# Kernel tuning notes

Measured on AMD Instinct MI355X. Metric: run time of the kernel, lower is better.

The kernel has to match this reference:

```python
import jax, jax.numpy as jnp
import numpy as np

D_MODEL = 1024
N_STATE = 16
D_INNER = 2 * D_MODEL          # 2048
DT_RANK = (D_MODEL + 15) // 16  # 64 = ceil(d/16)
K_CONV = 4
B, L = 1, 1024


def setup_inputs() -> dict:
    key = jax.random.key(0)
    ks = jax.random.split(key, 9)
    s = lambda fan_in: 1.0 / np.sqrt(fan_in)
    x = jax.random.normal(ks[0], (B, L, D_MODEL), dtype=jnp.float32)
    W_in = jax.random.normal(ks[1], (D_MODEL, 2 * D_INNER), dtype=jnp.float32) * s(D_MODEL)
    conv_w = jax.random.normal(ks[2], (D_INNER, K_CONV), dtype=jnp.float32) * s(K_CONV)
    conv_b = jnp.zeros((D_INNER,), dtype=jnp.float32)
    W_x = jax.random.normal(ks[3], (D_INNER, DT_RANK + 2 * N_STATE), dtype=jnp.float32) * s(D_INNER)
    W_dt = jax.random.normal(ks[4], (DT_RANK, D_INNER), dtype=jnp.float32) * s(DT_RANK)
    b_dt = jax.random.normal(ks[5], (D_INNER,), dtype=jnp.float32) * 0.01
    # A_log initialized as log(1..N) repeated over d_inner, as in __init__
    A_log = jnp.log(jnp.broadcast_to(jnp.arange(1, N_STATE + 1, dtype=jnp.float32), (D_INNER, N_STATE)))
    D = jnp.ones((D_INNER,), dtype=jnp.float32)
    W_out = jax.random.normal(ks[6], (D_INNER, D_MODEL), dtype=jnp.float32) * s(D_INNER)
    return {"x": x, "W_in": W_in, "conv_w": conv_w, "conv_b": conv_b,
            "W_x": W_x, "W_dt": W_dt, "b_dt": b_dt, "A_log": A_log,
            "D": D, "W_out": W_out}


def _causal_dw_conv(x, w, b):
    # x: [B,L,C], w: [C,K], b: [C]; causal depthwise conv (pad left K-1)
    K = w.shape[1]
    xp = jnp.pad(x, ((0, 0), (K - 1, 0), (0, 0)))
    Lx = x.shape[1]
    out = b
    for k in range(K):  # small fixed K=4
        out = out + xp[:, k:k + Lx, :] * w[:, k]
    return out


def _selective_scan(u, delta, A, Bm, Cm, D):
    # u,delta: [B,L,Di]; A: [Di,N]; Bm,Cm: [B,L,N]; D: [Di]
    dA = jnp.exp(delta[..., None] * A)                      # [B,L,Di,N]
    dBu = delta[..., None] * Bm[:, :, None, :] * u[..., None]
    dA_t = jnp.moveaxis(dA, 1, 0)    # [L,B,Di,N]
    dBu_t = jnp.moveaxis(dBu, 1, 0)
    C_t = jnp.moveaxis(Cm, 1, 0)     # [L,B,N]

    def step(h, inp):
        dA_i, dBu_i, C_i = inp
        h = dA_i * h + dBu_i
        y = jnp.einsum('bdn,bn->bd', h, C_i)
        return h, y

    h0 = jnp.zeros(u.shape[:1] + A.shape, dtype=u.dtype)  # [B,Di,N]
    _, ys = jax.lax.scan(step, h0, (dA_t, dBu_t, C_t))
    y = jnp.moveaxis(ys, 0, 1)       # [B,L,Di]
    return y + u * D


def reference(x, W_in, conv_w, conv_b, W_x, W_dt, b_dt, A_log, D, W_out):
    silu = jax.nn.silu
    x_and_res = x @ W_in                                   # [B,L,2*Di]
    x_in, res = jnp.split(x_and_res, 2, axis=-1)
    x_conv = silu(_causal_dw_conv(x_in, conv_w, conv_b))   # [B,L,Di]
    x_dbl = x_conv @ W_x                                   # [B,L,dt_rank+2N]
    dt, Bm, Cm = jnp.split(x_dbl, [DT_RANK, DT_RANK + N_STATE], axis=-1)
    delta = jax.nn.softplus(dt @ W_dt + b_dt)              # [B,L,Di]
    A = -jnp.exp(A_log)                                    # [Di,N]
    y = _selective_scan(x_conv, delta, A, Bm, Cm, D)
    return (y * silu(res)) @ W_out                         # [B,L,d_model]
```

## Files before the change

kernel.cpp:

```cpp
#include <hip/hip_runtime.h>

typedef unsigned short u16;
typedef unsigned int u32;
typedef __attribute__((ext_vector_type(8))) short bf16x8;
typedef __attribute__((ext_vector_type(4))) float f32x4;

#define LSEQ 1024
#define NSL 8

__device__ __forceinline__ float b2f(u16 v) { return __uint_as_float(((u32)v) << 16); }
__device__ __forceinline__ u16 f2b(float f) {
    u32 x = __float_as_uint(f);
    return (u16)((x + 0x7fffu + ((x >> 16) & 1u)) >> 16);
}
__device__ __forceinline__ float rdf(const void* p, size_t i, int f) {
    return f ? b2f(((const u16*)p)[i]) : ((const float*)p)[i];
}
__device__ __forceinline__ float fsig(float x) {
    return __builtin_amdgcn_rcpf(1.f + __expf(-x));
}

typedef const __attribute__((address_space(1))) u32* gp_t;
typedef __attribute__((address_space(3))) u32* lp_t;
__device__ __forceinline__ void gload16(const u16* g, u16* lds_wave_base) {
    __builtin_amdgcn_global_load_lds((gp_t)g, (lp_t)lds_wave_base, 16, 0, 0);
}

__global__ __launch_bounds__(256) void prep_k(const void* __restrict__ x,
                                              const void* __restrict__ W_in,
                                              const void* __restrict__ W_out,
                                              const void* __restrict__ W_x,
                                              const void* __restrict__ W_dt,
                                              u16* __restrict__ xb,
                                              u16* __restrict__ W_in_t,
                                              u16* __restrict__ W_out_t,
                                              u16* __restrict__ W_x_t,
                                              u16* __restrict__ W_dt_t,
                                              int* __restrict__ flag) {
    __shared__ int cnt;
    __shared__ __align__(8) u16 tile[32][36];
    if (threadIdx.x == 0) cnt = 0;
    __syncthreads();
    const u16* xu = (const u16*)x;
    int c = 0;
#pragma unroll
    for (int j = 0; j < 8; ++j) {
        u16 u = xu[threadIdx.x * 8 + j];
        int e = (u >> 7) & 0xFF;
        c += (e == 0 || (e >= 100 && e <= 140)) ? 1 : 0;
    }
    atomicAdd(&cnt, c);
    __syncthreads();
    const int f = (cnt >= 1638) ? 1 : 0;
    if (blockIdx.x == 0 && threadIdx.x == 0) *flag = f;

    int blk = blockIdx.x;
    if (blk < 1024) {
        int i = (blk * 256 + threadIdx.x) * 4;
        ushort4 o;
        if (f) {
            o = *(const ushort4*)(xu + i);
        } else {
            float4 v = *(const float4*)((const float*)x + i);
            o = make_ushort4(f2b(v.x), f2b(v.y), f2b(v.z), f2b(v.w));
        }
        *(ushort4*)(xb + i) = o;
        return;
    }
    blk -= 1024;
    const void* src; u16* dst; int R, Cn, nbc, t;
    if (blk < 4096)      { src = W_in;  dst = W_in_t;  R = 1024; Cn = 4096; nbc = 128; t = blk; }
    else if (blk < 6144) { src = W_out; dst = W_out_t; R = 2048; Cn = 1024; nbc = 32;  t = blk - 4096; }
    else if (blk < 6400) { src = W_x;   dst = W_x_t;   R = 2048; Cn = 96;   nbc = 4;   t = blk - 6144; }
    else                 { src = W_dt;  dst = W_dt_t;  R = 64;   Cn = 2048; nbc = 64;  t = blk - 6400; }
    int br = t / nbc, bc = t - br * nbc;
    int r0 = br * 32, c0 = bc * 32;
    {
        int ty = threadIdx.x >> 3, tx4 = (threadIdx.x & 7) << 2;
        u16 o0 = 0, o1 = 0, o2 = 0, o3 = 0;
        if (c0 + tx4 < Cn) {
            size_t off = (size_t)(r0 + ty) * Cn + c0 + tx4;
            if (f) {
                ushort4 u = *(const ushort4*)((const u16*)src + off);
                o0 = u.x; o1 = u.y; o2 = u.z; o3 = u.w;
            } else {
                float4 v = *(const float4*)((const float*)src + off);
                o0 = f2b(v.x); o1 = f2b(v.y); o2 = f2b(v.z); o3 = f2b(v.w);
            }
        }
        *(ushort4*)(&tile[ty][tx4]) = make_ushort4(o0, o1, o2, o3);
    }
    __syncthreads();
    {
        int cc = threadIdx.x >> 3, r4 = (threadIdx.x & 7) << 2;
        ushort4 o = make_ushort4(tile[r4][cc], tile[r4 + 1][cc], tile[r4 + 2][cc], tile[r4 + 3][cc]);
        *(ushort4*)(dst + (size_t)(c0 + cc) * R + r0 + r4) = o;
    }
}

template <int MT, int NT, int OUT_MODE>
__global__ __launch_bounds__(256) void gemm_bt(const u16* __restrict__ A,
                                               const u16* __restrict__ Bt,
                                               void* __restrict__ C,
                                               int M, int N, int K,
                                               const int* __restrict__ flag) {
    constexpr int BM = 32 * MT, BN = 32 * NT;
    __shared__ __align__(16) u16 As[2][2 * BM * 32];
    __shared__ __align__(16) u16 Bs[2][2 * BN * 32];
    const int tid = threadIdx.x;
    const int w = tid >> 6, lane = tid & 63;
    const int wm = w & 1, wn = w >> 1;
    const int m_blk = blockIdx.x * BM, n_blk = blockIdx.y * BN;
    const int lm = lane & 15, lq = lane >> 4;
    const int sr = lane >> 2, sc = (lane & 3) << 3;
    const int f = (OUT_MODE == 2) ? flag[0] : 0;

    f32x4 acc[MT][NT];
#pragma unroll
    for (int i = 0; i < MT; ++i)
#pragma unroll
        for (int j = 0; j < NT; ++j) acc[i][j] = (f32x4){0.f, 0.f, 0.f, 0.f};

    auto stage = [&](int buf, int kb) {
#pragma unroll
        for (int cch = 0; cch < 2; ++cch) {
#pragma unroll
            for (int i = 0; i < BM / 64; ++i) {
                int row = i * 64 + w * 16;
                gload16(A + (size_t)(m_blk + row + sr) * K + kb + cch * 32 + sc,
                        &As[buf][cch * BM * 32 + row * 32]);
            }
#pragma unroll
            for (int i = 0; i < BN / 64; ++i) {
                int row = i * 64 + w * 16;
                gload16(Bt + (size_t)(n_blk + row + sr) * K + kb + cch * 32 + sc,
                        &Bs[buf][cch * BN * 32 + row * 32]);
            }
        }
    };
    auto compute = [&](int buf) {
#pragma unroll
        for (int cch = 0; cch < 2; ++cch) {
            bf16x8 af[MT], bf[NT];
#pragma unroll
            for (int tm = 0; tm < MT; ++tm)
                af[tm] = *(const bf16x8*)(&As[buf][cch * BM * 32 +
                                                   (wm * 16 * MT + tm * 16 + lm) * 32 + lq * 8]);
#pragma unroll
            for (int tn = 0; tn < NT; ++tn)
                bf[tn] = *(const bf16x8*)(&Bs[buf][cch * BN * 32 +
                                                   (wn * 16 * NT + tn * 16 + lm) * 32 + lq * 8]);
#pragma unroll
            for (int tm = 0; tm < MT; ++tm)
#pragma unroll
                for (int tn = 0; tn < NT; ++tn)
                    acc[tm][tn] = __builtin_amdgcn_mfma_f32_16x16x32_bf16(af[tm], bf[tn],
                                                                          acc[tm][tn], 0, 0, 0);
        }
    };

    stage(0, 0);
    __syncthreads();
    int cur = 0;
    for (int kb = 64; kb < K; kb += 64) {
        stage(cur ^ 1, kb);
        compute(cur);
        __syncthreads();
        cur ^= 1;
    }
    compute(cur);

#pragma unroll
    for (int tm = 0; tm < MT; ++tm)
#pragma unroll
        for (int tn = 0; tn < NT; ++tn)
#pragma unroll
            for (int r = 0; r < 4; ++r) {
                int row = m_blk + wm * 16 * MT + tm * 16 + lq * 4 + r;
                int col = n_blk + wn * 16 * NT + tn * 16 + lm;
                float v = acc[tm][tn][r];
                if (OUT_MODE == 1) {
                    ((u16*)C)[(size_t)row * N + col] = f2b(v);
                } else {
                    if (f) ((u16*)C)[(size_t)row * N + col] = f2b(v);
                    else   ((float*)C)[(size_t)row * N + col] = v;
                }
            }
}

__global__ __launch_bounds__(256) void gemm2_conv_k(const u16* __restrict__ xz,
                                                    const u16* __restrict__ Bt,
                                                    float* __restrict__ parts,
                                                    u16* __restrict__ xconv,
                                                    const void* __restrict__ cw,
                                                    const void* __restrict__ cb,
                                                    const int* __restrict__ flag) {
    constexpr int MT = 2, NT = 4;
    constexpr int BM = 64, BN = 128, K = 2048, KLEN = 256;
    __shared__ __align__(16) u16 As[2][2 * BM * 32];
    __shared__ __align__(16) u16 Bs[2][2 * BN * 32];
    __shared__ __align__(16) float cws[KLEN * 4];
    __shared__ float cbs[KLEN];
    const int tid = threadIdx.x;
    const int w = tid >> 6, lane = tid & 63;
    const int wm = w & 1, wn = w >> 1;
    const int m_blk = blockIdx.x * BM;
    const int kb0 = blockIdx.z * KLEN;
    const int lm = lane & 15, lq = lane >> 4;
    const int sr = lane >> 2, sc = (lane & 3) << 3;
    const int f = flag[0];

    {
#pragma unroll
        for (int k = 0; k < 4; ++k) cws[tid * 4 + k] = rdf(cw, (size_t)(kb0 + tid) * 4 + k, f);
        cbs[tid] = rdf(cb, kb0 + tid, f);
    }
    __syncthreads();

    f32x4 acc[MT][NT];
#pragma unroll
    for (int i = 0; i < MT; ++i)
#pragma unroll
        for (int j = 0; j < NT; ++j) acc[i][j] = (f32x4){0.f, 0.f, 0.f, 0.f};

    const int arow = tid >> 2;
    const int acg = (tid & 3) << 3;
    const int trow = m_blk + arow;

    auto bstage = [&](int buf, int kb) {
#pragma unroll
        for (int cch = 0; cch < 2; ++cch)
#pragma unroll
            for (int i = 0; i < BN / 64; ++i) {
                int row = i * 64 + w * 16;
                gload16(Bt + (size_t)(row + sr) * K + kb + cch * 32 + sc,
                        &Bs[buf][cch * BN * 32 + row * 32]);
            }
    };
    auto astage = [&](int buf, int cch, int kbase) {
        const int d = kbase + acg;
        const int dl = kbase - kb0 + acg;
        bf16x8 xv[4];
#pragma unroll
        for (int kk = 0; kk < 4; ++kk) {
            bf16x8 zz = {0, 0, 0, 0, 0, 0, 0, 0};
            int tt = trow + kk - 3;
            xv[kk] = (tt >= 0) ? *(const bf16x8*)(xz + (size_t)tt * 4096 + d) : zz;
        }
        bf16x8 rv;
#pragma unroll
        for (int j = 0; j < 8; ++j) {
            f32x4 wv = *(const f32x4*)(cws + (dl + j) * 4);
            float a = cbs[dl + j];
#pragma unroll
            for (int kk = 0; kk < 4; ++kk) a += b2f((u16)xv[kk][j]) * wv[kk];
            rv[j] = (short)f2b(a * fsig(a));
        }
        *(bf16x8*)(&As[buf][cch * BM * 32 + arow * 32 + acg]) = rv;
        *(bf16x8*)(xconv + (size_t)trow * 2048 + d) = rv;
    };
    auto compute = [&](int buf) {
#pragma unroll
        for (int cch = 0; cch < 2; ++cch) {
            bf16x8 af[MT], bf[NT];
#pragma unroll
            for (int tm = 0; tm < MT; ++tm)
                af[tm] = *(const bf16x8*)(&As[buf][cch * BM * 32 +
                                                   (wm * 32 + tm * 16 + lm) * 32 + lq * 8]);
#pragma unroll
            for (int tn = 0; tn < NT; ++tn)
                bf[tn] = *(const bf16x8*)(&Bs[buf][cch * BN * 32 +
                                                   (wn * 64 + tn * 16 + lm) * 32 + lq * 8]);
#pragma unroll
            for (int tm = 0; tm < MT; ++tm)
#pragma unroll
                for (int tn = 0; tn < NT; ++tn)
                    acc[tm][tn] = __builtin_amdgcn_mfma_f32_16x16x32_bf16(af[tm], bf[tn],
                                                                          acc[tm][tn], 0, 0, 0);
        }
    };

    bstage(0, kb0);
    astage(0, 0, kb0);
    astage(0, 1, kb0 + 32);
    __syncthreads();
    int cur = 0;
    for (int kb = kb0 + 64; kb < kb0 + KLEN; kb += 64) {
        bstage(cur ^ 1, kb);
        astage(cur ^ 1, 0, kb);
        astage(cur ^ 1, 1, kb + 32);
        compute(cur);
        __syncthreads();
        cur ^= 1;
    }
    compute(cur);

#pragma unroll
    for (int tm = 0; tm < MT; ++tm)
#pragma unroll
        for (int tn = 0; tn < NT; ++tn)
#pragma unroll
            for (int r = 0; r < 4; ++r) {
                int row = m_blk + wm * 32 + tm * 16 + lq * 4 + r;
                int col = wn * 64 + tn * 16 + lm;
                parts[(size_t)blockIdx.z * 131072 + (size_t)row * 128 + col] = acc[tm][tn][r];
            }
}

__device__ __forceinline__ void delta_tile(const float* __restrict__ parts,
                                           const u16* __restrict__ Wdt,
                                           const void* __restrict__ bias,
                                           int f, int t0, int d0,
                                           u16* As2, u16* Bs2, float (*dlt)[128],
                                           int tid, int w, int lm, int lq, int sr, int sc) {
#pragma unroll
    for (int cch = 0; cch < 2; ++cch)
#pragma unroll
        for (int i = 0; i < 2; ++i) {
            int row = i * 64 + w * 16;
            gload16(Wdt + (size_t)(d0 + row + sr) * 64 + cch * 32 + sc,
                    Bs2 + cch * 4096 + row * 32);
        }
    {
        int arow = tid >> 3, acg = (tid & 7) << 3;
        f32x4 s0 = {0.f, 0.f, 0.f, 0.f}, s1 = {0.f, 0.f, 0.f, 0.f};
#pragma unroll
        for (int sl = 0; sl < NSL; ++sl) {
            const float* p = parts + (size_t)sl * 131072 + (size_t)(t0 + arow) * 128 + acg;
            s0 += *(const f32x4*)p;
            s1 += *(const f32x4*)(p + 4);
        }
        bf16x8 rv;
#pragma unroll
        for (int j = 0; j < 4; ++j) {
            rv[j] = (short)f2b(s0[j]);
            rv[4 + j] = (short)f2b(s1[j]);
        }
        *(bf16x8*)(As2 + (acg >> 5) * 1024 + arow * 32 + (acg & 31)) = rv;
    }
    __syncthreads();

    f32x4 dacc[2][2];
#pragma unroll
    for (int i = 0; i < 2; ++i)
#pragma unroll
        for (int j = 0; j < 2; ++j) dacc[i][j] = (f32x4){0.f, 0.f, 0.f, 0.f};
#pragma unroll
    for (int cch = 0; cch < 2; ++cch) {
        bf16x8 af[2], bf[2];
#pragma unroll
        for (int tm = 0; tm < 2; ++tm)
            af[tm] = *(const bf16x8*)(As2 + cch * 1024 + (tm * 16 + lm) * 32 + lq * 8);
#pragma unroll
        for (int tn = 0; tn < 2; ++tn)
            bf[tn] = *(const bf16x8*)(Bs2 + cch * 4096 + (w * 32 + tn * 16 + lm) * 32 + lq * 8);
#pragma unroll
        for (int tm = 0; tm < 2; ++tm)
#pragma unroll
            for (int tn = 0; tn < 2; ++tn)
                dacc[tm][tn] = __builtin_amdgcn_mfma_f32_16x16x32_bf16(af[tm], bf[tn],
                                                                       dacc[tm][tn], 0, 0, 0);
    }
#pragma unroll
    for (int tm = 0; tm < 2; ++tm)
#pragma unroll
        for (int tn = 0; tn < 2; ++tn)
#pragma unroll
            for (int r = 0; r < 4; ++r) {
                int row = tm * 16 + lq * 4 + r;
                int col = w * 32 + tn * 16 + lm;
                float b = rdf(bias, d0 + col, f);
                float t2 = dacc[tm][tn][r] + b;
                dlt[row][col] = fmaxf(t2, 0.f) + __logf(1.f + __expf(-fabsf(t2)));
            }
    __syncthreads();
}

__global__ __launch_bounds__(256) void scan1_k(const u16* __restrict__ xc,
                                               const float* __restrict__ parts,
                                               const u16* __restrict__ Wdt,
                                               const void* __restrict__ bias,
                                               const void* __restrict__ A_log,
                                               float* __restrict__ Acar,
                                               float* __restrict__ Bcar,
                                               const int* __restrict__ flag) {
    __shared__ __align__(16) u16 As2[2 * 32 * 32];
    __shared__ __align__(16) u16 Bs2[2 * 128 * 32];
    __shared__ float dlt[32][128];
    __shared__ float BCs[32][32];
    const int f = *flag;
    const int tid = threadIdx.x, b = blockIdx.x;
    const int w = tid >> 6, lane = tid & 63;
    const int lm = lane & 15, lq = lane >> 4;
    const int sr = lane >> 2, sc = (lane & 3) << 3;
    const int c = b >> 4;
    const int d0 = (b & 15) * 128;
    const int t0 = c * 32;
    {
        int idx = tid * 4;
        int tl = idx >> 5, col = idx & 31;
        f32x4 s = {0.f, 0.f, 0.f, 0.f};
#pragma unroll
        for (int sl = 0; sl < NSL; ++sl)
            s += *(const f32x4*)(parts + (size_t)sl * 131072 + (size_t)(t0 + tl) * 128 + 64 + col);
        *(f32x4*)&BCs[tl][col] = s;
    }
    delta_tile(parts, Wdt, bias, f, t0, d0, As2, Bs2, dlt, tid, w, lm, lq, sr, sc);

    const int dl = tid >> 1, nh = tid & 1;
    const int d = d0 + dl, n0 = nh << 3;
    float A[8], P[8], h[8];
#pragma unroll
    for (int j = 0; j < 8; ++j) {
        A[j] = -__expf(rdf(A_log, d * 16 + n0 + j, f));
        P[j] = 1.f;
        h[j] = 0.f;
    }
#pragma unroll 4
    for (int i = 0; i < 32; ++i) {
        int t = t0 + i;
        float de = dlt[i][dl];
        float dBu = de * b2f(xc[t * 2048 + d]);
        f32x4 Bv0 = *(const f32x4*)&BCs[i][n0];
        f32x4 Bv1 = *(const f32x4*)&BCs[i][n0 + 4];
#pragma unroll
        for (int j = 0; j < 8; ++j) {
            float Bv = (j < 4) ? Bv0[j & 3] : Bv1[j & 3];
            float a = __expf(de * A[j]);
            h[j] = a * h[j] + Bv * dBu;
            P[j] *= a;
        }
    }
    f32x4 pa0 = {P[0], P[1], P[2], P[3]}, pa1 = {P[4], P[5], P[6], P[7]};
    f32x4 hb0 = {h[0], h[1], h[2], h[3]}, hb1 = {h[4], h[5], h[6], h[7]};
    size_t base = (size_t)c * 32768 + d * 16 + n0;
    *(f32x4*)(Acar + base) = pa0;
    *(f32x4*)(Acar + base + 4) = pa1;
    *(f32x4*)(Bcar + base) = hb0;
    *(f32x4*)(Bcar + base + 4) = hb1;
}

__global__ __launch_bounds__(64) void scan2_k(const float* __restrict__ Acar,
                                              float* __restrict__ Bcar) {
    int idx = blockIdx.x * 64 + threadIdx.x;
    float a[32], b[32];
#pragma unroll
    for (int c = 0; c < 32; ++c) {
        a[c] = Acar[c * 32768 + idx];
        b[c] = Bcar[c * 32768 + idx];
    }
    float H = 0.f;
#pragma unroll
    for (int c = 0; c < 32; ++c) {
        float t = b[c];
        b[c] = H;
        H = a[c] * H + t;
    }
#pragma unroll
    for (int c = 0; c < 32; ++c) Bcar[c * 32768 + idx] = b[c];
}

__global__ __launch_bounds__(256) void scan3_k(const u16* __restrict__ xc,
                                               const float* __restrict__ parts,
                                               const u16* __restrict__ Wdt,
                                               const void* __restrict__ bias,
                                               const u16* __restrict__ xz,
                                               const void* __restrict__ A_log,
                                               const void* __restrict__ Dvp,
                                               const float* __restrict__ Bcar,
                                               u16* __restrict__ yg,
                                               const int* __restrict__ flag) {
    __shared__ __align__(16) u16 As2[2 * 32 * 32];
    __shared__ __align__(16) u16 Bs2[2 * 128 * 32];
    __shared__ float dlt[32][128];
    __shared__ float BCs[32][32];
    const int f = *flag;
    const int tid = threadIdx.x, b = blockIdx.x;
    const int w = tid >> 6, lane = tid & 63;
    const int lm = lane & 15, lq = lane >> 4;
    const int sr = lane >> 2, sc = (lane & 3) << 3;
    const int c = b >> 4;
    const int d0 = (b & 15) * 128;
    const int t0 = c * 32;
    {
        int idx = tid * 4;
        int tl = idx >> 5, col = idx & 31;
        f32x4 s = {0.f, 0.f, 0.f, 0.f};
#pragma unroll
        for (int sl = 0; sl < NSL; ++sl)
            s += *(const f32x4*)(parts + (size_t)sl * 131072 + (size_t)(t0 + tl) * 128 + 64 + col);
        *(f32x4*)&BCs[tl][col] = s;
    }
    delta_tile(parts, Wdt, bias, f, t0, d0, As2, Bs2, dlt, tid, w, lm, lq, sr, sc);

    const int dl = tid >> 1, nh = tid & 1;
    const int d = d0 + dl, n0 = nh << 3;
    float A[8], h[8];
    size_t base = (size_t)c * 32768 + d * 16 + n0;
    f32x4 h0 = *(const f32x4*)(Bcar + base);
    f32x4 h1 = *(const f32x4*)(Bcar + base + 4);
#pragma unroll
    for (int j = 0; j < 8; ++j) {
        A[j] = -__expf(rdf(A_log, d * 16 + n0 + j, f));
        h[j] = (j < 4) ? h0[j & 3] : h1[j & 3];
    }
    float Dd = rdf(Dvp, d, f);
#pragma unroll 4
    for (int i = 0; i < 32; ++i) {
        int t = t0 + i;
        float de = dlt[i][dl];
        float u = b2f(xc[t * 2048 + d]);
        float dBu = de * u;
        f32x4 Bv0 = *(const f32x4*)&BCs[i][n0];
        f32x4 Bv1 = *(const f32x4*)&BCs[i][n0 + 4];
        f32x4 Cv0 = *(const f32x4*)&BCs[i][16 + n0];
        f32x4 Cv1 = *(const f32x4*)&BCs[i][20 + n0];
        float p = 0.f;
#pragma unroll
        for (int j = 0; j < 8; ++j) {
            float Bv = (j < 4) ? Bv0[j & 3] : Bv1[j & 3];
            float Cv = (j < 4) ? Cv0[j & 3] : Cv1[j & 3];
            float a = __expf(de * A[j]);
            h[j] = a * h[j] + Bv * dBu;
            p += h[j] * Cv;
        }
        p += __shfl_xor(p, 1);
        if (nh == 0) {
            float r = b2f(xz[(size_t)t * 4096 + 2048 + d]);
            float yt = p + u * Dd;
            yg[t * 2048 + d] = f2b(yt * r * fsig(r));
        }
    }
}

__global__ __launch_bounds__(256) void gemm3_red_k(const float* __restrict__ parts,
                                                   const u16* __restrict__ Bt,
                                                   float* __restrict__ delta,
                                                   const void* __restrict__ bias,
                                                   const int* __restrict__ flag) {
    constexpr int MT = 2, NT = 2, BM = 64, BN = 64, K = 64;
    __shared__ __align__(16) u16 As[2 * BM * 32];
    __shared__ __align__(16) u16 Bs[2 * BN * 32];
    const int tid = threadIdx.x;
    const int w = tid >> 6, lane = tid & 63;
    const int wm = w & 1, wn = w >> 1;
    const int m_blk = blockIdx.x * BM, n_blk = blockIdx.y * BN;
    const int lm = lane & 15, lq = lane >> 4;
    const int sr = lane >> 2, sc = (lane & 3) << 3;
    const int f = flag[0];

    f32x4 acc[MT][NT];
#pragma unroll
    for (int i = 0; i < MT; ++i)
#pragma unroll
        for (int j = 0; j < NT; ++j) acc[i][j] = (f32x4){0.f, 0.f, 0.f, 0.f};

    const int arow = tid >> 2;
    const int acg = (tid & 3) << 3;

#pragma unroll
    for (int cch = 0; cch < 2; ++cch) {
        int row = w * 16;
        gload16(Bt + (size_t)(n_blk + row + sr) * K + cch * 32 + sc, &Bs[cch * BN * 32 + row * 32]);
    }
#pragma unroll
    for (int cch = 0; cch < 2; ++cch) {
        f32x4 s0 = {0.f, 0.f, 0.f, 0.f}, s1 = {0.f, 0.f, 0.f, 0.f};
#pragma unroll
        for (int sl = 0; sl < NSL; ++sl) {
            const float* p = parts + (size_t)sl * 131072 + (size_t)(m_blk + arow) * 128 + cch * 32 + acg;
            s0 += *(const f32x4*)p;
            s1 += *(const f32x4*)(p + 4);
        }
        bf16x8 rv;
#pragma unroll
        for (int j = 0; j < 4; ++j) {
            rv[j] = (short)f2b(s0[j]);
            rv[4 + j] = (short)f2b(s1[j]);
        }
        *(bf16x8*)(&As[cch * BM * 32 + arow * 32 + acg]) = rv;
    }
    __syncthreads();

#pragma unroll
    for (int cch = 0; cch < 2; ++cch) {
        bf16x8 af[MT], bf[NT];
#pragma unroll
        for (int tm = 0; tm < MT; ++tm)
            af[tm] = *(const bf16x8*)(&As[cch * BM * 32 + (wm * 32 + tm * 16 + lm) * 32 + lq * 8]);
#pragma unroll
        for (int tn = 0; tn < NT; ++tn)
            bf[tn] = *(const bf16x8*)(&Bs[cch * BN * 32 + (wn * 32 + tn * 16 + lm) * 32 + lq * 8]);
#pragma unroll
        for (int tm = 0; tm < MT; ++tm)
#pragma unroll
            for (int tn = 0; tn < NT; ++tn)
                acc[tm][tn] = __builtin_amdgcn_mfma_f32_16x16x32_bf16(af[tm], bf[tn],
                                                                      acc[tm][tn], 0, 0, 0);
    }

#pragma unroll
    for (int tm = 0; tm < MT; ++tm)
#pragma unroll
        for (int tn = 0; tn < NT; ++tn)
#pragma unroll
            for (int r = 0; r < 4; ++r) {
                int row = m_blk + wm * 32 + tm * 16 + lq * 4 + r;
                int col = n_blk + wn * 32 + tn * 16 + lm;
                float b = rdf(bias, col, f);
                float t2 = acc[tm][tn][r] + b;
                float sp = fmaxf(t2, 0.f) + __logf(1.f + __expf(-fabsf(t2)));
                delta[(size_t)row * 2048 + col] = sp;
            }
}

__global__ __launch_bounds__(256) void scan_k(const float* __restrict__ delta,
                                              const u16* __restrict__ xc,
                                              const float* __restrict__ parts,
                                              const u16* __restrict__ xz,
                                              const void* __restrict__ A_log,
                                              const void* __restrict__ Dvp,
                                              u16* __restrict__ yg,
                                              const int* __restrict__ flag) {
    int f = *flag;
    int g = blockIdx.x * 256 + threadIdx.x;
    int d = g >> 4, n = g & 15;
    float A = -__expf(rdf(A_log, d * 16 + n, f));
    float Dd = rdf(Dvp, d, f);
    float h = 0.f;
    for (int t = 0; t < LSEQ; ++t) {
        float de = delta[t * 2048 + d];
        float u = b2f(xc[t * 2048 + d]);
        float Bv = 0.f, Cv = 0.f;
#pragma unroll
        for (int sl = 0; sl < NSL; ++sl) {
            Bv += parts[(size_t)sl * 131072 + (size_t)t * 128 + 64 + n];
            Cv += parts[(size_t)sl * 131072 + (size_t)t * 128 + 80 + n];
        }
        h = __expf(de * A) * h + (de * Bv) * u;
        float p = h * Cv;
        p += __shfl_xor(p, 1);
        p += __shfl_xor(p, 2);
        p += __shfl_xor(p, 4);
        p += __shfl_xor(p, 8);
        if (n == 0) {
            float r = b2f(xz[(size_t)t * 4096 + 2048 + d]);
            float yt = p + u * Dd;
            yg[t * 2048 + d] = f2b(yt * r * fsig(r));
        }
    }
}

extern "C" void kernel_launch(void* const* d_in, const int* in_sizes, int n_in,
                              void* d_out, int out_size, void* d_ws, size_t ws_size,
                              hipStream_t stream) {
    const void* x      = d_in[0];
    const void* W_in   = d_in[1];
    const void* conv_w = d_in[2];
    const void* conv_b = d_in[3];
    const void* W_x    = d_in[4];
    const void* W_dt   = d_in[5];
    const void* b_dt   = d_in[6];
    const void* A_log  = d_in[7];
    const void* Dv     = d_in[8];
    const void* W_out  = d_in[9];

    char* ws = (char*)d_ws;
    u16*   xz     = (u16*)(ws);
    u16*   xconv  = (u16*)(ws + 8388608);
    float* parts  = (float*)(ws + 12582912);
    u16*   W_in_t = (u16*)(ws + 16777216);
    u16*   yg     = (u16*)(ws + 25165824);
    u16*   xb     = (u16*)(ws + 25165824);
    u16*   W_x_t  = (u16*)(ws + 29360128);
    u16*   W_dt_t = (u16*)(ws + 29884416);
    u16*   W_out_t= (u16*)(ws + 30146560);
    int*   flag   = (int*)(ws + 34340864);
    float* Acar   = (float*)(ws + 34340992);
    float* Bcar   = (float*)(ws + 38535296);
    float* dfb    = (float*)(ws + 34340992);
    const bool chunked_ok = (ws_size >= 42729600);

    prep_k<<<7552, 256, 0, stream>>>(x, W_in, W_out, W_x, W_dt,
                                     xb, W_in_t, W_out_t, W_x_t, W_dt_t, flag);
    gemm_bt<2, 4, 1><<<dim3(16, 32), 256, 0, stream>>>(xb, W_in_t, (void*)xz,
                                                       1024, 4096, 1024, flag);
    gemm2_conv_k<<<dim3(16, 1, 8), 256, 0, stream>>>(xz, W_x_t, parts, xconv,
                                                     conv_w, conv_b, flag);

    if (chunked_ok) {
        scan1_k<<<512, 256, 0, stream>>>(xconv, parts, W_dt_t, b_dt, A_log, Acar, Bcar, flag);
        scan2_k<<<512, 64, 0, stream>>>(Acar, Bcar);
        scan3_k<<<512, 256, 0, stream>>>(xconv, parts, W_dt_t, b_dt, xz, A_log, Dv,
                                         Bcar, yg, flag);
    } else {
        gemm3_red_k<<<dim3(16, 32), 256, 0, stream>>>(parts, W_dt_t, dfb, b_dt, flag);
        scan_k<<<128, 256, 0, stream>>>(dfb, xconv, parts, xz, A_log, Dv, yg, flag);
    }

    gemm_bt<2, 2, 2><<<dim3(16, 16), 256, 0, stream>>>(yg, W_out_t, d_out,
                                                       1024, 1024, 2048, flag);
}
```

Measured before the change: 210.6 us.

## Fuse three-pass chunked scan into one kernel with inter-block flag handoff

Replaces the scan1/scan2/scan3 launches with a single kernel. Each block computes its chunk's decay product and partial state and publishes them with a release flag. It then spins until all earlier chunks for the same channel block are published, combines their carries serially, and runs the output pass. This removes two launches and the recomputation of the delta tile and BC sums in the third pass. In exchange it relies on blocks being scheduled in an order that avoids deadlock, and later chunks serially combine up to 31 prior carries from global memory.

```diff
diff --git a/kernel.cpp b/kernel.cpp
--- a/kernel.cpp
+++ b/kernel.cpp
@@ -36,6 +36,7 @@
                                               u16* __restrict__ W_out_t,
                                               u16* __restrict__ W_x_t,
                                               u16* __restrict__ W_dt_t,
+                                              int* __restrict__ scan_flags,
                                               int* __restrict__ flag) {
     __shared__ int cnt;
     __shared__ __align__(8) u16 tile[32][36];
@@ -56,6 +57,10 @@
 
     int blk = blockIdx.x;
     if (blk < 1024) {
+        if (blk == 0) {
+            scan_flags[threadIdx.x] = 0;
+            scan_flags[256 + threadIdx.x] = 0;
+        }
         int i = (blk * 256 + threadIdx.x) * 4;
         ushort4 o;
         if (f) {
@@ -376,14 +381,18 @@
     __syncthreads();
 }
 
-__global__ __launch_bounds__(256) void scan1_k(const u16* __restrict__ xc,
-                                               const float* __restrict__ parts,
-                                               const u16* __restrict__ Wdt,
-                                               const void* __restrict__ bias,
-                                               const void* __restrict__ A_log,
-                                               float* __restrict__ Acar,
-                                               float* __restrict__ Bcar,
-                                               const int* __restrict__ flag) {
+__global__ __launch_bounds__(256) void scan_fused_k(const u16* __restrict__ xc,
+                                                    const float* __restrict__ parts,
+                                                    const u16* __restrict__ Wdt,
+                                                    const void* __restrict__ bias,
+                                                    const u16* __restrict__ xz,
+                                                    const void* __restrict__ A_log,
+                                                    const void* __restrict__ Dvp,
+                                                    float* __restrict__ Acar,
+                                                    float* __restrict__ Bcar,
+                                                    int* __restrict__ flags,
+                                                    u16* __restrict__ yg,
+                                                    const int* __restrict__ flag) {
     __shared__ __align__(16) u16 As2[2 * 32 * 32];
     __shared__ __align__(16) u16 Bs2[2 * 128 * 32];
     __shared__ float dlt[32][128];
@@ -393,8 +402,8 @@
     const int w = tid >> 6, lane = tid & 63;
     const int lm = lane & 15, lq = lane >> 4;
     const int sr = lane >> 2, sc = (lane & 3) << 3;
-    const int c = b >> 4;
-    const int d0 = (b & 15) * 128;
+    const int c = b >> 4, dblk = b & 15;
+    const int d0 = dblk * 128;
     const int t0 = c * 32;
     {
         int idx = tid * 4;
@@ -409,6 +418,7 @@
 
     const int dl = tid >> 1, nh = tid & 1;
     const int d = d0 + dl, n0 = nh << 3;
+
     float A[8], P[8], h[8];
 #pragma unroll
     for (int j = 0; j < 8; ++j) {
@@ -431,79 +441,45 @@
             P[j] *= a;
         }
     }
-    f32x4 pa0 = {P[0], P[1], P[2], P[3]}, pa1 = {P[4], P[5], P[6], P[7]};
-    f32x4 hb0 = {h[0], h[1], h[2], h[3]}, hb1 = {h[4], h[5], h[6], h[7]};
     size_t base = (size_t)c * 32768 + d * 16 + n0;
-    *(f32x4*)(Acar + base) = pa0;
-    *(f32x4*)(Acar + base + 4) = pa1;
-    *(f32x4*)(Bcar + base) = hb0;
-    *(f32x4*)(Bcar + base + 4) = hb1;
-}
-
-__global__ __launch_bounds__(64) void scan2_k(const float* __restrict__ Acar,
-                                              float* __restrict__ Bcar) {
-    int idx = blockIdx.x * 64 + threadIdx.x;
-    float a[32], b[32];
-#pragma unroll
-    for (int c = 0; c < 32; ++c) {
-        a[c] = Acar[c * 32768 + idx];
-        b[c] = Bcar[c * 32768 + idx];
-    }
-    float H = 0.f;
-#pragma unroll
-    for (int c = 0; c < 32; ++c) {
-        float t = b[c];
-        b[c] = H;
-        H = a[c] * H + t;
-    }
-#pragma unroll
-    for (int c = 0; c < 32; ++c) Bcar[c * 32768 + idx] = b[c];
-}
-
-__global__ __launch_bounds__(256) void scan3_k(const u16* __restrict__ xc,
-                                               const float* __restrict__ parts,
-                                               const u16* __restrict__ Wdt,
-                                               const void* __restrict__ bias,
-                                               const u16* __restrict__ xz,
-                                               const void* __restrict__ A_log,
-                                               const void* __restrict__ Dvp,
-                                               const float* __restrict__ Bcar,
-                                               u16* __restrict__ yg,
-                                               const int* __restrict__ flag) {
-    __shared__ __align__(16) u16 As2[2 * 32 * 32];
-    __shared__ __align__(16) u16 Bs2[2 * 128 * 32];
-    __shared__ float dlt[32][128];
-    __shared__ float BCs[32][32];
-    const int f = *flag;
-    const int tid = threadIdx.x, b = blockIdx.x;
-    const int w = tid >> 6, lane = tid & 63;
-    const int lm = lane & 15, lq = lane >> 4;
-    const int sr = lane >> 2, sc = (lane & 3) << 3;
-    const int c = b >> 4;
-    const int d0 = (b & 15) * 128;
-    const int t0 = c * 32;
     {
-        int idx = tid * 4;
-        int tl = idx >> 5, col = idx & 31;
-        f32x4 s = {0.f, 0.f, 0.f, 0.f};
-#pragma unroll
-        for (int sl = 0; sl < NSL; ++sl)
-            s += *(const f32x4*)(parts + (size_t)sl * 131072 + (size_t)(t0 + tl) * 128 + 64 + col);
-        *(f32x4*)&BCs[tl][col] = s;
-    }
-    delta_tile(parts, Wdt, bias, f, t0, d0, As2, Bs2, dlt, tid, w, lm, lq, sr, sc);
-
-    const int dl = tid >> 1, nh = tid & 1;
-    const int d = d0 + dl, n0 = nh << 3;
-    float A[8], h[8];
-    size_t base = (size_t)c * 32768 + d * 16 + n0;
-    f32x4 h0 = *(const f32x4*)(Bcar + base);
-    f32x4 h1 = *(const f32x4*)(Bcar + base + 4);
-#pragma unroll
-    for (int j = 0; j < 8; ++j) {
-        A[j] = -__expf(rdf(A_log, d * 16 + n0 + j, f));
-        h[j] = (j < 4) ? h0[j & 3] : h1[j & 3];
-    }
+        f32x4 pa0 = {P[0], P[1], P[2], P[3]}, pa1 = {P[4], P[5], P[6], P[7]};
+        f32x4 hb0 = {h[0], h[1], h[2], h[3]}, hb1 = {h[4], h[5], h[6], h[7]};
+        *(f32x4*)(Acar + base) = pa0;
+        *(f32x4*)(Acar + base + 4) = pa1;
+        *(f32x4*)(Bcar + base) = hb0;
+        *(f32x4*)(Bcar + base + 4) = hb1;
+    }
+    __syncthreads();
+    if (tid == 0)
+        __hip_atomic_store(&flags[b], 1, __ATOMIC_RELEASE, __HIP_MEMORY_SCOPE_AGENT);
+
+    float H[8];
+#pragma unroll
+    for (int j = 0; j < 8; ++j) H[j] = 0.f;
+    if (c > 0) {
+        if (tid < c) {
+            while (__hip_atomic_load(&flags[tid * 16 + dblk], __ATOMIC_ACQUIRE,
+                                     __HIP_MEMORY_SCOPE_AGENT) == 0)
+                __builtin_amdgcn_s_sleep(1);
+        }
+        __syncthreads();
+        for (int cc = 0; cc < c; ++cc) {
+            size_t cb = (size_t)cc * 32768 + d * 16 + n0;
+            f32x4 a0 = *(const f32x4*)(Acar + cb);
+            f32x4 a1 = *(const f32x4*)(Acar + cb + 4);
+            f32x4 b0 = *(const f32x4*)(Bcar + cb);
+            f32x4 b1 = *(const f32x4*)(Bcar + cb + 4);
+#pragma unroll
+            for (int j = 0; j < 4; ++j) {
+                H[j] = a0[j] * H[j] + b0[j];
+                H[4 + j] = a1[j] * H[4 + j] + b1[j];
+            }
+        }
+    }
+
+#pragma unroll
+    for (int j = 0; j < 8; ++j) h[j] = H[j];
     float Dd = rdf(Dvp, d, f);
 #pragma unroll 4
     for (int i = 0; i < 32; ++i) {
@@ -678,21 +654,20 @@
     int*   flag   = (int*)(ws + 34340864);
     float* Acar   = (float*)(ws + 34340992);
     float* Bcar   = (float*)(ws + 38535296);
+    int*   sflags = (int*)(ws + 42729600);
     float* dfb    = (float*)(ws + 34340992);
-    const bool chunked_ok = (ws_size >= 42729600);
+    const bool chunked_ok = (ws_size >= 42731648);
 
     prep_k<<<7552, 256, 0, stream>>>(x, W_in, W_out, W_x, W_dt,
-                                     xb, W_in_t, W_out_t, W_x_t, W_dt_t, flag);
+                                     xb, W_in_t, W_out_t, W_x_t, W_dt_t, sflags, flag);
     gemm_bt<2, 4, 1><<<dim3(16, 32), 256, 0, stream>>>(xb, W_in_t, (void*)xz,
                                                        1024, 4096, 1024, flag);
     gemm2_conv_k<<<dim3(16, 1, 8), 256, 0, stream>>>(xz, W_x_t, parts, xconv,
                                                      conv_w, conv_b, flag);
 
     if (chunked_ok) {
-        scan1_k<<<512, 256, 0, stream>>>(xconv, parts, W_dt_t, b_dt, A_log, Acar, Bcar, flag);
-        scan2_k<<<512, 64, 0, stream>>>(Acar, Bcar);
-        scan3_k<<<512, 256, 0, stream>>>(xconv, parts, W_dt_t, b_dt, xz, A_log, Dv,
-                                         Bcar, yg, flag);
+        scan_fused_k<<<512, 256, 0, stream>>>(xconv, parts, W_dt_t, b_dt, xz, A_log, Dv,
+                                              Acar, Bcar, sflags, yg, flag);
     } else {
         gemm3_red_k<<<dim3(16, 32), 256, 0, stream>>>(parts, W_dt_t, dfb, b_dt, flag);
         scan_k<<<128, 256, 0, stream>>>(dfb, xconv, parts, xz, A_log, Dv, yg, flag);
```

After: 224.2 us. 6.4% more time.
